# Kernel tuning notes

Hardware: AMD Instinct MI355X
Metric: run time of the kernel (lower is better)

## Reference

```python
import jax, jax.numpy as jnp
import numpy as np

NUM_POS = 4
N = 8192
C = 4096  # number of identity classes == logit dim


def setup_inputs() -> dict:
    key = jax.random.key(0)
    k1, k2 = jax.random.split(key)
    feat = jax.random.normal(k1, (N, C), dtype=jnp.float32)
    label = jax.random.randint(k2, (N,), 0, C, dtype=jnp.int64)
    return {"feat": feat, "label": label}


def reference(feat, label):
    # feat: [n, C] logits, label: [n] int class ids.
    n, c = feat.shape
    # Segment-mean replaces the O(n^2) masked-mean loop:
    # center[i] = mean of feat over all j with label[j] == label[i]
    sums = jax.ops.segment_sum(feat, label, num_segments=c)              # [C, C]
    counts = jax.ops.segment_sum(jnp.ones((n,), feat.dtype), label,
                                 num_segments=c)                          # [C]
    center = sums[label] / counts[label][:, None]                         # [n, C]
    # CrossEntropyLoss (mean reduction) on centers as logits
    logp = jax.nn.log_softmax(center, axis=-1)
    ce = -jnp.take_along_axis(logp, label[:, None], axis=1)[:, 0].mean()
    m = n / NUM_POS
    return ce / m
```

## Files before the change

### kernel.cpp

```cpp
#include <hip/hip_runtime.h>
#include <math.h>

#define NN 8192
#define CC 4096
#define SLOTS 64
#define BLK 256

#define SCALE (4.0f / (8192.0f * 8192.0f))

__global__ void init_kernel(int* __restrict__ counts) {
    int i = blockIdx.x * blockDim.x + threadIdx.x;
    if (i < CC) counts[i] = 0;
}

__global__ void build_index(const int* __restrict__ label,
                            int* __restrict__ counts,
                            int* __restrict__ lists) {
    int i = blockIdx.x * blockDim.x + threadIdx.x;
    if (i < NN) {
        int lab = label[i];
        int pos = atomicAdd(&counts[lab], 1);
        if (pos < SLOTS) lists[lab * SLOTS + pos] = i;
    }
}

__global__ __launch_bounds__(BLK) void class_loss(const float* __restrict__ feat,
                                                  const int* __restrict__ counts,
                                                  const int* __restrict__ lists,
                                                  float* __restrict__ value) {
    int c = blockIdx.x;
    int t = threadIdx.x;

    __shared__ int s_cnt;
    __shared__ int s_rows[SLOTS];
    if (t == 0) s_cnt = counts[c];
    if (t < SLOTS) s_rows[t] = lists[c * SLOTS + t];
    __syncthreads();

    int cnt = s_cnt;
    if (cnt == 0) {
        if (t == 0) value[c] = 0.0f;
        return;
    }

    float4 acc[4];
    #pragma unroll
    for (int j = 0; j < 4; ++j) acc[j] = make_float4(0.f, 0.f, 0.f, 0.f);

    int m = cnt < SLOTS ? cnt : SLOTS;
    for (int k = 0; k < m; ++k) {
        const float4* rowp = (const float4*)(feat + (size_t)s_rows[k] * CC);
        #pragma unroll
        for (int j = 0; j < 4; ++j) {
            float4 v = rowp[j * 256 + t];
            acc[j].x += v.x; acc[j].y += v.y; acc[j].z += v.z; acc[j].w += v.w;
        }
    }

    float inv = 1.0f / (float)cnt;
    float vals[16];
    #pragma unroll
    for (int j = 0; j < 4; ++j) {
        vals[j * 4 + 0] = acc[j].x * inv;
        vals[j * 4 + 1] = acc[j].y * inv;
        vals[j * 4 + 2] = acc[j].z * inv;
        vals[j * 4 + 3] = acc[j].w * inv;
    }

    __shared__ float s_red[4];
    __shared__ float s_bcast;
    __shared__ float s_vc;

    float wm = vals[0];
    #pragma unroll
    for (int j = 1; j < 16; ++j) wm = fmaxf(wm, vals[j]);
    #pragma unroll
    for (int off = 32; off > 0; off >>= 1) wm = fmaxf(wm, __shfl_down(wm, off, 64));
    int lane = t & 63, wv = t >> 6;
    if (lane == 0) s_red[wv] = wm;
    __syncthreads();
    if (t == 0) s_bcast = fmaxf(fmaxf(s_red[0], s_red[1]), fmaxf(s_red[2], s_red[3]));
    __syncthreads();
    float M = s_bcast;

    float se = 0.f;
    #pragma unroll
    for (int j = 0; j < 16; ++j) se += expf(vals[j] - M);
    #pragma unroll
    for (int off = 32; off > 0; off >>= 1) se += __shfl_down(se, off, 64);
    if (lane == 0) s_red[wv] = se;

    if (t == ((c & 1023) >> 2)) s_vc = vals[((c >> 10) << 2) | (c & 3)];
    __syncthreads();

    if (t == 0) {
        float S = s_red[0] + s_red[1] + s_red[2] + s_red[3];
        float v = M + logf(S) - s_vc;
        value[c] = (float)cnt * v;
    }
}

__global__ __launch_bounds__(BLK) void finalize(const float* __restrict__ value,
                                                float* __restrict__ out) {
    int t = threadIdx.x;
    const float4* v4 = (const float4*)value;
    float s = 0.f;
    #pragma unroll
    for (int i = 0; i < CC / 4 / BLK; ++i) {
        float4 v = v4[i * BLK + t];
        s += v.x + v.y + v.z + v.w;
    }
    #pragma unroll
    for (int off = 32; off > 0; off >>= 1) s += __shfl_down(s, off, 64);
    __shared__ float s_red[4];
    int lane = t & 63, wv = t >> 6;
    if (lane == 0) s_red[wv] = s;
    __syncthreads();
    if (t == 0) out[0] = (s_red[0] + s_red[1] + s_red[2] + s_red[3]) * SCALE;
}

extern "C" void kernel_launch(void* const* d_in, const int* in_sizes, int n_in,
                              void* d_out, int out_size, void* d_ws, size_t ws_size,
                              hipStream_t stream) {
    const float* feat = (const float*)d_in[0];
    const int* label = (const int*)d_in[1];
    float* out = (float*)d_out;

    int* counts = (int*)d_ws;
    int* lists = counts + CC;
    float* value = (float*)(lists + CC * SLOTS);

    init_kernel<<<(CC + BLK - 1) / BLK, BLK, 0, stream>>>(counts);
    build_index<<<(NN + BLK - 1) / BLK, BLK, 0, stream>>>(label, counts, lists);
    class_loss<<<CC, BLK, 0, stream>>>(feat, counts, lists, value);
    finalize<<<1, BLK, 0, stream>>>(value, out);
}
```

Before: 201.6 us.

## Map one class per wavefront and drop block-level shared reductions

Reorganizes class_loss so each 64-lane wave owns one class, with four classes per block. Row indices are broadcast via shuffles and all reductions are wave-local xor shuffles, removing shared memory and __syncthreads barriers. Each lane now holds 16 float4 accumulators, raising register pressure and possibly lowering occupancy. Fast __expf/__logf intrinsics replace the precise versions.

```diff
diff --git a/kernel.cpp b/kernel.cpp
--- a/kernel.cpp
+++ b/kernel.cpp
@@ -5,6 +5,7 @@
 #define CC 4096
 #define SLOTS 64
 #define BLK 256
+#define WPB 4
 
 #define SCALE (4.0f / (8192.0f * 8192.0f))
 
@@ -28,76 +29,69 @@
                                                   const int* __restrict__ counts,
                                                   const int* __restrict__ lists,
                                                   float* __restrict__ value) {
-    int c = blockIdx.x;
-    int t = threadIdx.x;
+    int lane = threadIdx.x & 63;
+    int wave = threadIdx.x >> 6;
+    int c = blockIdx.x * WPB + wave;
 
-    __shared__ int s_cnt;
-    __shared__ int s_rows[SLOTS];
-    if (t == 0) s_cnt = counts[c];
-    if (t < SLOTS) s_rows[t] = lists[c * SLOTS + t];
-    __syncthreads();
+    int cnt = counts[c];
+    int r_lane = lists[c * SLOTS + lane];
+    int m = cnt < SLOTS ? cnt : SLOTS;
 
-    int cnt = s_cnt;
+    float4 a[16];
+    #pragma unroll
+    for (int i = 0; i < 16; ++i) a[i] = make_float4(0.f, 0.f, 0.f, 0.f);
+
+    for (int k = 0; k < m; ++k) {
+        int r = __shfl(r_lane, k, 64);
+        const float4* rowp = (const float4*)(feat + (size_t)r * CC);
+        #pragma unroll
+        for (int i = 0; i < 16; ++i) {
+            float4 v = rowp[i * 64 + lane];
+            a[i].x += v.x; a[i].y += v.y; a[i].z += v.z; a[i].w += v.w;
+        }
+    }
+
     if (cnt == 0) {
-        if (t == 0) value[c] = 0.0f;
+        if (lane == 0) value[c] = 0.0f;
         return;
     }
 
-    float4 acc[4];
+    float inv = 1.0f / (float)cnt;
+
+    float wm = -INFINITY;
     #pragma unroll
-    for (int j = 0; j < 4; ++j) acc[j] = make_float4(0.f, 0.f, 0.f, 0.f);
+    for (int i = 0; i < 16; ++i) {
+        a[i].x *= inv; a[i].y *= inv; a[i].z *= inv; a[i].w *= inv;
+        wm = fmaxf(wm, fmaxf(fmaxf(a[i].x, a[i].y), fmaxf(a[i].z, a[i].w)));
+    }
+    #pragma unroll
+    for (int off = 1; off < 64; off <<= 1)
+        wm = fmaxf(wm, __shfl_xor(wm, off, 64));
+    float M = wm;
 
-    int m = cnt < SLOTS ? cnt : SLOTS;
-    for (int k = 0; k < m; ++k) {
-        const float4* rowp = (const float4*)(feat + (size_t)s_rows[k] * CC);
-        #pragma unroll
-        for (int j = 0; j < 4; ++j) {
-            float4 v = rowp[j * 256 + t];
-            acc[j].x += v.x; acc[j].y += v.y; acc[j].z += v.z; acc[j].w += v.w;
+    int ci = c >> 8;
+    int cj = c & 3;
+    bool mylane = (lane == ((c >> 2) & 63));
+    float se = 0.f, vc = 0.f;
+    #pragma unroll
+    for (int i = 0; i < 16; ++i) {
+        se += __expf(a[i].x - M);
+        se += __expf(a[i].y - M);
+        se += __expf(a[i].z - M);
+        se += __expf(a[i].w - M);
+        if (mylane && i == ci) {
+            float v = (cj == 0) ? a[i].x : (cj == 1) ? a[i].y : (cj == 2) ? a[i].z : a[i].w;
+            vc += v;
         }
     }
-
-    float inv = 1.0f / (float)cnt;
-    float vals[16];
     #pragma unroll
-    for (int j = 0; j < 4; ++j) {
-        vals[j * 4 + 0] = acc[j].x * inv;
-        vals[j * 4 + 1] = acc[j].y * inv;
-        vals[j * 4 + 2] = acc[j].z * inv;
-        vals[j * 4 + 3] = acc[j].w * inv;
+    for (int off = 1; off < 64; off <<= 1) {
+        se += __shfl_xor(se, off, 64);
+        vc += __shfl_xor(vc, off, 64);
     }
 
-    __shared__ float s_red[4];
-    __shared__ float s_bcast;
-    __shared__ float s_vc;
-
-    float wm = vals[0];
-    #pragma unroll
-    for (int j = 1; j < 16; ++j) wm = fmaxf(wm, vals[j]);
-    #pragma unroll
-    for (int off = 32; off > 0; off >>= 1) wm = fmaxf(wm, __shfl_down(wm, off, 64));
-    int lane = t & 63, wv = t >> 6;
-    if (lane == 0) s_red[wv] = wm;
-    __syncthreads();
-    if (t == 0) s_bcast = fmaxf(fmaxf(s_red[0], s_red[1]), fmaxf(s_red[2], s_red[3]));
-    __syncthreads();
-    float M = s_bcast;
-
-    float se = 0.f;
-    #pragma unroll
-    for (int j = 0; j < 16; ++j) se += expf(vals[j] - M);
-    #pragma unroll
-    for (int off = 32; off > 0; off >>= 1) se += __shfl_down(se, off, 64);
-    if (lane == 0) s_red[wv] = se;
-
-    if (t == ((c & 1023) >> 2)) s_vc = vals[((c >> 10) << 2) | (c & 3)];
-    __syncthreads();
-
-    if (t == 0) {
-        float S = s_red[0] + s_red[1] + s_red[2] + s_red[3];
-        float v = M + logf(S) - s_vc;
-        value[c] = (float)cnt * v;
-    }
+    if (lane == 0)
+        value[c] = (float)cnt * (M + __logf(se) - vc);
 }
 
 __global__ __launch_bounds__(BLK) void finalize(const float* __restrict__ value,
@@ -111,7 +105,7 @@
         s += v.x + v.y + v.z + v.w;
     }
     #pragma unroll
-    for (int off = 32; off > 0; off >>= 1) s += __shfl_down(s, off, 64);
+    for (int off = 1; off < 64; off <<= 1) s += __shfl_xor(s, off, 64);
     __shared__ float s_red[4];
     int lane = t & 63, wv = t >> 6;
     if (lane == 0) s_red[wv] = s;
@@ -132,6 +126,6 @@
 
     init_kernel<<<(CC + BLK - 1) / BLK, BLK, 0, stream>>>(counts);
     build_index<<<(NN + BLK - 1) / BLK, BLK, 0, stream>>>(label, counts, lists);
-    class_loss<<<CC, BLK, 0, stream>>>(feat, counts, lists, value);
+    class_loss<<<CC / WPB, BLK, 0, stream>>>(feat, counts, lists, value);
     finalize<<<1, BLK, 0, stream>>>(value, out);
 }
```

Measured after the change: 202.6 us. No clear change (+0.5%).
